# Optimization experiments

Hardware: AMD Instinct MI355X
Metric: run time of the kernel (lower is better)

Reference implementation:

```python
import jax, jax.numpy as jnp
import numpy as np

EMB = 1024
HID = 4 * EMB
HEADS = 16
HEAD_DIM = EMB // HEADS


def gelu_tanh(x):
    c = jnp.sqrt(jnp.asarray(2.0 / jnp.pi, x.dtype))
    return 0.5 * x * (1.0 + jnp.tanh(c * (x + 0.044715 * x ** 3)))


def layernorm(x, scale, shift, eps=1e-5):
    mean = jnp.mean(x, axis=-1, keepdims=True)
    var = jnp.var(x, axis=-1, keepdims=True)
    return scale * (x - mean) / jnp.sqrt(var + eps) + shift


def setup_inputs() -> dict:
    key = jax.random.key(0)
    ks = jax.random.split(key, 12)
    s = 0.02
    return {
        "x": jax.random.normal(ks[0], (2, 2048, EMB), jnp.float32),
        "Wq": jax.random.normal(ks[1], (EMB, EMB), jnp.float32) * s,
        "Wk": jax.random.normal(ks[2], (EMB, EMB), jnp.float32) * s,
        "Wv": jax.random.normal(ks[3], (EMB, EMB), jnp.float32) * s,
        "Wo": jax.random.normal(ks[4], (EMB, EMB), jnp.float32) * s,
        "bo": jnp.zeros((EMB,), jnp.float32),
        "W1": jax.random.normal(ks[5], (EMB, HID), jnp.float32) * s,
        "b1": jnp.zeros((HID,), jnp.float32),
        "W2": jax.random.normal(ks[6], (HID, EMB), jnp.float32) * s,
        "b2": jnp.zeros((EMB,), jnp.float32),
        "ln1_scale": jnp.ones((EMB,), jnp.float32),
        "ln1_shift": jnp.zeros((EMB,), jnp.float32),
        "ln2_scale": jnp.ones((EMB,), jnp.float32),
        "ln2_shift": jnp.zeros((EMB,), jnp.float32),
    }


def reference(x, Wq, Wk, Wv, Wo, bo, W1, b1, W2, b2,
              ln1_scale, ln1_shift, ln2_scale, ln2_shift):
    B, S, D = x.shape

    # pre-norm attention + residual
    h = layernorm(x, ln1_scale, ln1_shift)
    q = (h @ Wq).reshape(B, S, HEADS, HEAD_DIM).transpose(0, 2, 1, 3)  # bhsd
    k = (h @ Wk).reshape(B, S, HEADS, HEAD_DIM).transpose(0, 2, 1, 3)
    v = (h @ Wv).reshape(B, S, HEADS, HEAD_DIM).transpose(0, 2, 1, 3)

    scores = jnp.einsum("bhqd,bhkd->bhqk", q, k)
    causal = jnp.tril(jnp.ones((S, S), bool))
    scores = jnp.where(causal, scores, -jnp.inf)
    attn = jax.nn.softmax(scores / jnp.sqrt(jnp.asarray(HEAD_DIM, x.dtype)), axis=-1)
    ctx = jnp.einsum("bhqk,bhkd->bhqd", attn, v)
    ctx = ctx.transpose(0, 2, 1, 3).reshape(B, S, D)
    x = x + (ctx @ Wo + bo)

    # pre-norm FFN + residual
    h = layernorm(x, ln2_scale, ln2_shift)
    h = gelu_tanh(h @ W1 + b1) @ W2 + b2
    return x + h
```

## Files before the change

kernel.cpp:

```cpp
#include <hip/hip_runtime.h>
#include <hip/hip_bf16.h>
#include <stdint.h>

#define B_   2
#define S_   2048
#define D_   1024
#define H_   16
#define DH_  64
#define HID_ 4096
#define M_   4096

typedef __bf16 bf16x8 __attribute__((ext_vector_type(8)));
typedef float  f32x4  __attribute__((ext_vector_type(4)));

typedef const uint32_t __attribute__((address_space(1))) u32g;
typedef uint32_t       __attribute__((address_space(3))) u32l;

__device__ __forceinline__ uint16_t f2bf(float f) {
  uint32_t u = __builtin_bit_cast(uint32_t, f);
  u += 0x7FFFu + ((u >> 16) & 1u);
  return (uint16_t)(u >> 16);
}

__device__ __forceinline__ float bf2f(uint16_t u) {
  return __builtin_bit_cast(float, (uint32_t)u << 16);
}

__device__ __forceinline__ void gload_lds16(const void* g, void* l) {
  __builtin_amdgcn_global_load_lds((u32g*)g, (u32l*)l, 16, 0, 0);
}

__device__ __forceinline__ const bf16x8* lds8p(const uint16_t* base, int row,
                                               int cole) {
  int byt = (cole * 2) ^ ((row & 7) << 4);
  return reinterpret_cast<const bf16x8*>(base + row * 64 + (byt >> 1));
}

__global__ void wconv_t(const float* __restrict__ W, uint16_t* __restrict__ WT,
                        int K, int N) {
  __shared__ float tile[32][33];
  int n0 = blockIdx.x * 32, k0 = blockIdx.y * 32;
  int tx = threadIdx.x, ty = threadIdx.y;
#pragma unroll
  for (int i = 0; i < 4; ++i)
    tile[ty + i * 8][tx] = W[(size_t)(k0 + ty + i * 8) * N + n0 + tx];
  __syncthreads();
#pragma unroll
  for (int i = 0; i < 4; ++i)
    WT[(size_t)(n0 + ty + i * 8) * K + k0 + tx] = f2bf(tile[tx][ty + i * 8]);
}

__global__ __launch_bounds__(256) void ln_k(const float* __restrict__ x,
                                            const float* __restrict__ sc,
                                            const float* __restrict__ sh,
                                            uint16_t* __restrict__ out) {
  int row = blockIdx.x;
  int t = threadIdx.x;
  float4 v = reinterpret_cast<const float4*>(x + (size_t)row * D_)[t];
  float s = v.x + v.y + v.z + v.w;
  float ss = v.x * v.x + v.y * v.y + v.z * v.z + v.w * v.w;
#pragma unroll
  for (int off = 32; off >= 1; off >>= 1) {
    s += __shfl_xor(s, off);
    ss += __shfl_xor(ss, off);
  }
  __shared__ float red[8];
  int wid = t >> 6, lane = t & 63;
  if (lane == 0) { red[wid] = s; red[wid + 4] = ss; }
  __syncthreads();
  s = red[0] + red[1] + red[2] + red[3];
  ss = red[4] + red[5] + red[6] + red[7];
  float mean = s * (1.0f / D_);
  float var = ss * (1.0f / D_) - mean * mean;
  float rstd = rsqrtf(var + 1e-5f);
  float4 g = reinterpret_cast<const float4*>(sc)[t];
  float4 b = reinterpret_cast<const float4*>(sh)[t];
  ushort4 o;
  o.x = f2bf(g.x * (v.x - mean) * rstd + b.x);
  o.y = f2bf(g.y * (v.y - mean) * rstd + b.y);
  o.z = f2bf(g.z * (v.z - mean) * rstd + b.z);
  o.w = f2bf(g.w * (v.w - mean) * rstd + b.w);
  reinterpret_cast<ushort4*>(out + (size_t)row * D_)[t] = o;
}

__global__ __launch_bounds__(256) void reduce4_k(
    const uint16_t* __restrict__ P0, const uint16_t* __restrict__ P1,
    const uint16_t* __restrict__ P2, const uint16_t* __restrict__ P3,
    const float* __restrict__ resid, const float* __restrict__ bias,
    float* __restrict__ out) {
  int row = blockIdx.x, t = threadIdx.x;
  size_t base = (size_t)row * D_ + t * 4;
  float4 r = *reinterpret_cast<const float4*>(resid + base);
  float4 b = reinterpret_cast<const float4*>(bias)[t];
  ushort4 u0 = *reinterpret_cast<const ushort4*>(P0 + base);
  ushort4 u1 = *reinterpret_cast<const ushort4*>(P1 + base);
  ushort4 u2 = *reinterpret_cast<const ushort4*>(P2 + base);
  ushort4 u3 = *reinterpret_cast<const ushort4*>(P3 + base);
  float4 o;
  o.x = r.x + b.x + bf2f(u0.x) + bf2f(u1.x) + bf2f(u2.x) + bf2f(u3.x);
  o.y = r.y + b.y + bf2f(u0.y) + bf2f(u1.y) + bf2f(u2.y) + bf2f(u3.y);
  o.z = r.z + b.z + bf2f(u0.z) + bf2f(u1.z) + bf2f(u2.z) + bf2f(u3.z);
  o.w = r.w + b.w + bf2f(u0.w) + bf2f(u1.w) + bf2f(u2.w) + bf2f(u3.w);
  *reinterpret_cast<float4*>(out + base) = o;
}

__global__ void vtrans_k(const uint16_t* __restrict__ V, uint16_t* __restrict__ VT) {
  __shared__ uint16_t tile[32][33];
  int s0 = blockIdx.x * 32, d0 = blockIdx.y * 32, bh = blockIdx.z;
  int tx = threadIdx.x, ty = threadIdx.y;
  const uint16_t* vb = V + (size_t)bh * S_ * DH_;
  uint16_t* vtb = VT + (size_t)bh * DH_ * S_;
#pragma unroll
  for (int i = 0; i < 4; ++i)
    tile[ty + i * 8][tx] = vb[(size_t)(s0 + ty + i * 8) * DH_ + d0 + tx];
  __syncthreads();
#pragma unroll
  for (int i = 0; i < 4; ++i)
    vtb[(size_t)(d0 + ty + i * 8) * S_ + s0 + tx] = tile[tx][ty + i * 8];
}

template <int EPI>
__global__ __launch_bounds__(512, 2) void gemm8(
    const uint16_t* __restrict__ A, const uint16_t* __restrict__ BT,
    void* __restrict__ Cout, const float* __restrict__ bias,
    uint16_t* __restrict__ P0, uint16_t* __restrict__ P1,
    uint16_t* __restrict__ P2, uint16_t* __restrict__ P3,
    int M, int N, int K) {
  __shared__ uint16_t As[2][2][128 * 64];
  __shared__ uint16_t Bs[2][2][128 * 64];
  int t = threadIdx.x;
  int lane = t & 63, wid = t >> 6;
  int wm = wid >> 2, wn = wid & 3;
  int l15 = lane & 15, lk8 = (lane >> 4) * 8, lr4 = (lane >> 4) * 4;
  int gx = gridDim.x;
  int nwg = gx * gridDim.y;
  int bid = blockIdx.y * gx + blockIdx.x;
  int swz = (bid & 7) * (nwg >> 3) + (bid >> 3);
  int bx = swz % gx, by = swz / gx;
  int m0 = by * 256, n0 = bx * 256;
  int ksz = K / gridDim.z;
  int kbeg = blockIdx.z * ksz;
  int NT = ksz >> 6;

  int r0 = t >> 3, slot0 = t & 7;
  int scol = (slot0 ^ (r0 & 7)) * 8;

  auto STAGE_A = [&](int kt, int half, int buf) {
    const uint16_t* src =
        A + (size_t)(m0 + half * 128 + r0) * K + kbeg + kt * 64 + scol;
    uint16_t* dst = &As[buf][half][t * 8];
    gload_lds16(src, dst);
    gload_lds16(src + (size_t)64 * K, dst + 4096);
  };
  auto STAGE_B = [&](int kt, int half, int buf) {
    const uint16_t* src =
        BT + (size_t)(n0 + half * 128 + r0) * K + kbeg + kt * 64 + scol;
    uint16_t* dst = &Bs[buf][half][t * 8];
    gload_lds16(src, dst);
    gload_lds16(src + (size_t)64 * K, dst + 4096);
  };

  bf16x8 a[4][2], b[2][2];
  auto LDA = [&](int buf, int mh) {
#pragma unroll
    for (int j = 0; j < 4; ++j)
#pragma unroll
      for (int kk = 0; kk < 2; ++kk)
        a[j][kk] = *lds8p(As[buf][mh], wm * 64 + j * 16 + l15, kk * 32 + lk8);
  };
  auto LDB = [&](int buf, int nh) {
#pragma unroll
    for (int jj = 0; jj < 2; ++jj)
#pragma unroll
      for (int kk = 0; kk < 2; ++kk)
        b[jj][kk] = *lds8p(Bs[buf][nh], wn * 32 + jj * 16 + l15, kk * 32 + lk8);
  };

  f32x4 acc[8][4] = {};
  auto MM = [&](int mh, int nh) {
    __builtin_amdgcn_s_setprio(1);
#pragma unroll
    for (int kk = 0; kk < 2; ++kk)
#pragma unroll
      for (int j = 0; j < 4; ++j)
#pragma unroll
        for (int jj = 0; jj < 2; ++jj)
          acc[mh * 4 + j][nh * 2 + jj] = __builtin_amdgcn_mfma_f32_16x16x32_bf16(
              a[j][kk], b[jj][kk], acc[mh * 4 + j][nh * 2 + jj], 0, 0, 0);
    __builtin_amdgcn_s_setprio(0);
  };
  auto BAR = [&]() {
    __builtin_amdgcn_s_barrier();
    asm volatile("" ::: "memory");
  };
  auto LGKM0 = [&]() {
    asm volatile("s_waitcnt lgkmcnt(0)" ::: "memory");
    __builtin_amdgcn_sched_barrier(0);
  };

  STAGE_A(0, 0, 0);
  STAGE_B(0, 1, 0);
  STAGE_B(0, 0, 0);
  STAGE_A(0, 1, 0);
  STAGE_A(1, 0, 1);
  STAGE_B(1, 1, 1);
  asm volatile("s_waitcnt vmcnt(4)" ::: "memory");
  BAR();

  for (int T = 0; T < NT; ++T) {
    int cur = T & 1;
    LDA(cur, 0);
    LDB(cur, 0);
    if (T + 1 < NT) STAGE_B(T + 1, 0, cur ^ 1);
    BAR(); LGKM0();
    MM(0, 0);
    BAR();
    LDB(cur, 1);
    if (T + 1 < NT) STAGE_A(T + 1, 1, cur ^ 1);
    BAR(); LGKM0();
    MM(0, 1);
    BAR();
    LDA(cur, 1);
    if (T + 2 < NT) STAGE_A(T + 2, 0, cur);
    BAR(); LGKM0();
    MM(1, 1);
    BAR();
    LDB(cur, 0);
    if (T + 2 < NT) STAGE_B(T + 2, 1, cur);
    BAR(); LGKM0();
    MM(1, 0);
    if (T + 1 < NT) {
      if (T == NT - 2) {
        asm volatile("s_waitcnt vmcnt(0)" ::: "memory");
      } else {
        asm volatile("s_waitcnt vmcnt(4)" ::: "memory");
      }
    }
    BAR();
  }

  uint16_t* Pz = nullptr;
  if constexpr (EPI == 3) {
    int z = blockIdx.z;
    Pz = (z == 0) ? P0 : (z == 1) ? P1 : (z == 2) ? P2 : P3;
  }
#pragma unroll
  for (int mi = 0; mi < 8; ++mi) {
#pragma unroll
    for (int ni = 0; ni < 4; ++ni) {
#pragma unroll
      for (int rr = 0; rr < 4; ++rr) {
        int gm = m0 + (mi >> 2) * 128 + wm * 64 + (mi & 3) * 16 + lr4 + rr;
        int gn = n0 + (ni >> 1) * 128 + wn * 32 + (ni & 1) * 16 + l15;
        float v = acc[mi][ni][rr];
        if constexpr (EPI == 0) {
          int which = gn >> 10, nc = gn & 1023;
          int h = nc >> 6, dh = nc & 63;
          int bb = gm >> 11, s = gm & 2047;
          ((uint16_t*)Cout)[((size_t)which * 32 + bb * 16 + h) * (S_ * 64) +
                            (size_t)s * 64 + dh] = f2bf(v);
        } else if constexpr (EPI == 2) {
          float u = v + bias[gn];
          float y = 0.7978845608028654f * (u + 0.044715f * u * u * u);
          float e = __expf(2.0f * y);
          float th = 1.0f - 2.0f / (e + 1.0f);
          ((uint16_t*)Cout)[(size_t)gm * N + gn] = f2bf(0.5f * u * (1.0f + th));
        } else {
          Pz[(size_t)gm * N + gn] = f2bf(v);
        }
      }
    }
  }
}

template <int EPI>
__global__ __launch_bounds__(256) void gemm_bt(
    const uint16_t* __restrict__ A, const uint16_t* __restrict__ BT,
    void* __restrict__ Cout, const float* __restrict__ bias,
    const float* __restrict__ resid, int M, int N, int K) {
  __shared__ uint16_t Asm_[128 * 64];
  __shared__ uint16_t Bsm_[128 * 64];
  int t = threadIdx.x;
  int lane = t & 63, wid = t >> 6;
  int wr = wid >> 1, wc = wid & 1;
  int nwg = gridDim.x * gridDim.y;
  int bid = blockIdx.y * gridDim.x + blockIdx.x;
  int swz = (bid & 7) * (nwg >> 3) + (bid >> 3);
  int bx = swz % gridDim.x, by = swz / gridDim.x;
  int m0 = by * 128, n0 = bx * 128;
  int l15 = lane & 15, lk8 = (lane >> 4) * 8;
  f32x4 acc[4][4] = {};

  auto STAGE = [&](int k0) {
#pragma unroll
    for (int it = 0; it < 4; ++it) {
      int idx = it * 256 + t;
      int r = idx >> 3, slot = idx & 7;
      int c = (slot ^ (r & 7)) * 8;
      gload_lds16(A + (size_t)(m0 + r) * K + k0 + c, &Asm_[idx * 8]);
      gload_lds16(BT + (size_t)(n0 + r) * K + k0 + c, &Bsm_[idx * 8]);
    }
  };

  int niter = K >> 6;
  for (int ki = 0; ki < niter; ++ki) {
    __syncthreads();
    STAGE(ki * 64);
    __syncthreads();
#pragma unroll
    for (int kk = 0; kk < 2; ++kk) {
      bf16x8 a[4], b[4];
#pragma unroll
      for (int mi = 0; mi < 4; ++mi)
        a[mi] = *lds8p(Asm_, wr * 64 + mi * 16 + l15, kk * 32 + lk8);
#pragma unroll
      for (int ni = 0; ni < 4; ++ni)
        b[ni] = *lds8p(Bsm_, wc * 64 + ni * 16 + l15, kk * 32 + lk8);
#pragma unroll
      for (int mi = 0; mi < 4; ++mi)
#pragma unroll
        for (int ni = 0; ni < 4; ++ni)
          acc[mi][ni] = __builtin_amdgcn_mfma_f32_16x16x32_bf16(
              a[mi], b[ni], acc[mi][ni], 0, 0, 0);
    }
  }
  int lr4 = (lane >> 4) * 4;
#pragma unroll
  for (int mi = 0; mi < 4; ++mi) {
#pragma unroll
    for (int ni = 0; ni < 4; ++ni) {
#pragma unroll
      for (int r = 0; r < 4; ++r) {
        int gm = m0 + wr * 64 + mi * 16 + lr4 + r;
        int gn = n0 + wc * 64 + ni * 16 + l15;
        float v = acc[mi][ni][r];
        if constexpr (EPI == 1) {
          ((float*)Cout)[(size_t)gm * N + gn] =
              resid[(size_t)gm * N + gn] + v + bias[gn];
        }
      }
    }
  }
}

__global__ __launch_bounds__(256) void attn_k(const uint16_t* __restrict__ Q,
                                              const uint16_t* __restrict__ Kv,
                                              const uint16_t* __restrict__ VT,
                                              uint16_t* __restrict__ ctx) {
  __shared__ uint16_t Ksm[2][64 * 64];
  __shared__ uint16_t Vsm[2][64 * 64];
  __shared__ uint16_t Psm[4][16 * 64];
  int bh = blockIdx.y;
  int t = threadIdx.x, lane = t & 63, wid = t >> 6;
  int l15 = lane & 15, lk8 = (lane >> 4) * 8, lr4 = (lane >> 4) * 4;

  auto STAGE = [&](int kt, int bufi) {
    int k0 = kt * 64;
#pragma unroll
    for (int it = 0; it < 2; ++it) {
      int idx = it * 256 + t;
      int r = idx >> 3, slot = idx & 7;
      int c = (slot ^ (r & 7)) * 8;
      gload_lds16(Kv + ((size_t)bh * S_ + k0 + r) * 64 + c, &Ksm[bufi][idx * 8]);
      gload_lds16(VT + ((size_t)bh * 64 + r) * S_ + k0 + c, &Vsm[bufi][idx * 8]);
    }
  };

  for (int half = 0; half < 2; ++half) {
    int qt = half ? 31 - blockIdx.x : blockIdx.x;
    int q0 = qt * 64;
    bf16x8 qf[2];
#pragma unroll
    for (int kk = 0; kk < 2; ++kk)
      qf[kk] = *reinterpret_cast<const bf16x8*>(
          &Q[((size_t)bh * S_ + q0 + wid * 16 + l15) * 64 + kk * 32 + lk8]);
    f32x4 o[4] = {};
    float mrow[4], lsum[4];
#pragma unroll
    for (int r = 0; r < 4; ++r) { mrow[r] = -3.0e38f; lsum[r] = 0.0f; }

    int nkt = qt + 1;
    STAGE(0, 0);
    for (int kt = 0; kt < nkt; ++kt) {
      int cur = kt & 1;
      if (kt + 1 < nkt) {
        STAGE(kt + 1, cur ^ 1);
        asm volatile("s_waitcnt vmcnt(4)" ::: "memory");
      } else {
        asm volatile("s_waitcnt vmcnt(0)" ::: "memory");
      }
      __builtin_amdgcn_s_barrier();
      asm volatile("" ::: "memory");
      __builtin_amdgcn_sched_barrier(0);
      const uint16_t* Kb = Ksm[cur];
      const uint16_t* Vb = Vsm[cur];

      f32x4 sf[4] = {};
#pragma unroll
      for (int kk = 0; kk < 2; ++kk)
#pragma unroll
        for (int nt = 0; nt < 4; ++nt) {
          bf16x8 kb = *lds8p(Kb, nt * 16 + l15, kk * 32 + lk8);
          sf[nt] = __builtin_amdgcn_mfma_f32_16x16x32_bf16(qf[kk], kb, sf[nt], 0, 0, 0);
        }
      float sv[4][4];
      if (kt == qt) {
#pragma unroll
        for (int nt = 0; nt < 4; ++nt)
#pragma unroll
          for (int r = 0; r < 4; ++r) {
            float s = sf[nt][r] * 0.125f;
            int key = nt * 16 + l15;
            int qr = wid * 16 + lr4 + r;
            sv[nt][r] = (key <= qr) ? s : -3.0e38f;
          }
      } else {
#pragma unroll
        for (int nt = 0; nt < 4; ++nt)
#pragma unroll
          for (int r = 0; r < 4; ++r) sv[nt][r] = sf[nt][r] * 0.125f;
      }
      float pmax[4];
#pragma unroll
      for (int r = 0; r < 4; ++r)
        pmax[r] = fmaxf(fmaxf(sv[0][r], sv[1][r]), fmaxf(sv[2][r], sv[3][r]));
#pragma unroll
      for (int off = 8; off >= 1; off >>= 1)
#pragma unroll
        for (int r = 0; r < 4; ++r)
          pmax[r] = fmaxf(pmax[r], __shfl_xor(pmax[r], off));
      float fac[4];
#pragma unroll
      for (int r = 0; r < 4; ++r) {
        float mn = fmaxf(mrow[r], pmax[r]);
        fac[r] = __expf(mrow[r] - mn);
        mrow[r] = mn;
        lsum[r] *= fac[r];
      }
#pragma unroll
      for (int dt = 0; dt < 4; ++dt)
#pragma unroll
        for (int r = 0; r < 4; ++r) o[dt][r] *= fac[r];
      float psum[4] = {0.0f, 0.0f, 0.0f, 0.0f};
#pragma unroll
      for (int nt = 0; nt < 4; ++nt)
#pragma unroll
        for (int r = 0; r < 4; ++r) {
          float p = __expf(sv[nt][r] - mrow[r]);
          psum[r] += p;
          int prow = lr4 + r, pcol = nt * 16 + l15;
          Psm[wid][prow * 64 + ((((pcol * 2) ^ ((prow & 7) << 4))) >> 1)] = f2bf(p);
        }
#pragma unroll
      for (int off = 8; off >= 1; off >>= 1)
#pragma unroll
        for (int r = 0; r < 4; ++r) psum[r] += __shfl_xor(psum[r], off);
#pragma unroll
      for (int r = 0; r < 4; ++r) lsum[r] += psum[r];
#pragma unroll
      for (int kk = 0; kk < 2; ++kk) {
        bf16x8 pa = *lds8p(Psm[wid], l15, kk * 32 + lk8);
#pragma unroll
        for (int dt = 0; dt < 4; ++dt) {
          bf16x8 vb = *lds8p(Vb, dt * 16 + l15, kk * 32 + lk8);
          o[dt] = __builtin_amdgcn_mfma_f32_16x16x32_bf16(pa, vb, o[dt], 0, 0, 0);
        }
      }
      asm volatile("s_waitcnt lgkmcnt(0)" ::: "memory");
      __builtin_amdgcn_sched_barrier(0);
      __builtin_amdgcn_s_barrier();
      asm volatile("" ::: "memory");
    }
    int b = bh >> 4, h = bh & 15;
#pragma unroll
    for (int dt = 0; dt < 4; ++dt)
#pragma unroll
      for (int r = 0; r < 4; ++r) {
        int s = q0 + wid * 16 + lr4 + r;
        int dh = dt * 16 + l15;
        ctx[((size_t)(b * S_ + s)) * D_ + h * 64 + dh] = f2bf(o[dt][r] / lsum[r]);
      }
  }
}

extern "C" void kernel_launch(void* const* d_in, const int* in_sizes, int n_in,
                              void* d_out, int out_size, void* d_ws, size_t ws_size,
                              hipStream_t stream) {
  const float* x    = (const float*)d_in[0];
  const float* Wq   = (const float*)d_in[1];
  const float* Wk   = (const float*)d_in[2];
  const float* Wv   = (const float*)d_in[3];
  const float* Wo   = (const float*)d_in[4];
  const float* bo   = (const float*)d_in[5];
  const float* W1   = (const float*)d_in[6];
  const float* b1   = (const float*)d_in[7];
  const float* W2   = (const float*)d_in[8];
  const float* b2   = (const float*)d_in[9];
  const float* ln1s = (const float*)d_in[10];
  const float* ln1b = (const float*)d_in[11];
  const float* ln2s = (const float*)d_in[12];
  const float* ln2b = (const float*)d_in[13];
  float* out = (float*)d_out;
  char* ws = (char*)d_ws;

  const size_t MB = 1024 * 1024;
  uint16_t* WQKVT = (uint16_t*)(ws + 0);
  uint16_t* WOT   = (uint16_t*)(ws + 6 * MB);
  uint16_t* W1T   = (uint16_t*)(ws + 8 * MB);
  uint16_t* W2T   = (uint16_t*)(ws + 16 * MB);
  uint16_t* H1    = (uint16_t*)(ws + 24 * MB);
  float*    X1    = (float*)(ws + 32 * MB);
  uint16_t* QKV   = (uint16_t*)(ws + 48 * MB);
  uint16_t* VTb   = (uint16_t*)(ws + 72 * MB);
  uint16_t* CTX   = (uint16_t*)(ws + 80 * MB);
  uint16_t* FFH   = (uint16_t*)(ws + 48 * MB);
  uint16_t* SP0   = (uint16_t*)(ws + 0);
  uint16_t* SP1   = (uint16_t*)(ws + 8 * MB);
  uint16_t* SP2   = (uint16_t*)(ws + 24 * MB);
  uint16_t* SP3   = (uint16_t*)(ws + 80 * MB);

  dim3 b32x8(32, 8);
  wconv_t<<<dim3(32, 32), b32x8, 0, stream>>>(Wq, WQKVT, 1024, 1024);
  wconv_t<<<dim3(32, 32), b32x8, 0, stream>>>(Wk, WQKVT + 1024 * 1024, 1024, 1024);
  wconv_t<<<dim3(32, 32), b32x8, 0, stream>>>(Wv, WQKVT + 2 * 1024 * 1024, 1024, 1024);
  wconv_t<<<dim3(32, 32), b32x8, 0, stream>>>(Wo, WOT, 1024, 1024);
  wconv_t<<<dim3(128, 32), b32x8, 0, stream>>>(W1, W1T, 1024, 4096);
  wconv_t<<<dim3(32, 128), b32x8, 0, stream>>>(W2, W2T, 4096, 1024);

  ln_k<<<M_, 256, 0, stream>>>(x, ln1s, ln1b, H1);
  gemm8<0><<<dim3(12, 16), 512, 0, stream>>>(H1, WQKVT, QKV, nullptr,
                                             nullptr, nullptr, nullptr, nullptr,
                                             M_, 3072, 1024);
  const uint16_t* Qp = QKV;
  const uint16_t* Kp = QKV + (size_t)32 * S_ * 64;
  const uint16_t* Vp = QKV + (size_t)64 * S_ * 64;
  vtrans_k<<<dim3(64, 2, 32), b32x8, 0, stream>>>(Vp, VTb);
  attn_k<<<dim3(16, 32), 256, 0, stream>>>(Qp, Kp, VTb, CTX);
  gemm_bt<1><<<dim3(8, 32), 256, 0, stream>>>(CTX, WOT, X1, bo, x, M_, 1024, 1024);
  ln_k<<<M_, 256, 0, stream>>>(X1, ln2s, ln2b, H1);
  gemm8<2><<<dim3(16, 16), 512, 0, stream>>>(H1, W1T, FFH, b1,
                                             nullptr, nullptr, nullptr, nullptr,
                                             M_, 4096, 1024);
  gemm8<3><<<dim3(4, 16, 4), 512, 0, stream>>>(FFH, W2T, nullptr, nullptr,
                                               SP0, SP1, SP2, SP3,
                                               M_, 1024, 4096);
  reduce4_k<<<M_, 256, 0, stream>>>(SP0, SP1, SP2, SP3, X1, b2, out);
}
```

Baseline: 265.5 us.

## Rewrite attention as single-wave 32x32 MFMA kernel with register-resident P

Replaces the 4-wave, 64-row-tile attention kernel with a one-wave-per-block kernel over 32-query tiles using 32x32x16 MFMAs. S is computed transposed so each lane owns one query column, and P is packed to bf16 and moved between half-waves with cvt_pk and permlane32_swap instead of going through LDS. The softmax scale and log2(e) are folded into K in the QKV GEMM epilogue so the kernel can use exp2 directly. The running-max rescale is skipped unless the max grows by more than 8. The changes aim to cut LDS traffic, barriers and per-element exp/scale work, and to raise block count for load balance, at the cost of less K/V reuse per block.

```diff
diff --git a/kernel.cpp b/kernel.cpp
--- a/kernel.cpp
+++ b/kernel.cpp
@@ -12,9 +12,13 @@
 
 typedef __bf16 bf16x8 __attribute__((ext_vector_type(8)));
 typedef float  f32x4  __attribute__((ext_vector_type(4)));
+typedef float  f32x16 __attribute__((ext_vector_type(16)));
+typedef uint32_t u32x4v __attribute__((ext_vector_type(4)));
 
 typedef const uint32_t __attribute__((address_space(1))) u32g;
 typedef uint32_t       __attribute__((address_space(3))) u32l;
+
+#define SCL2K_ 0.18033688011112042f
 
 __device__ __forceinline__ uint16_t f2bf(float f) {
   uint32_t u = __builtin_bit_cast(uint32_t, f);
@@ -34,6 +38,15 @@
                                                int cole) {
   int byt = (cole * 2) ^ ((row & 7) << 4);
   return reinterpret_cast<const bf16x8*>(base + row * 64 + (byt >> 1));
+}
+
+__device__ __forceinline__ uint32_t cvtpk_bf16(float lo, float hi) {
+  uint32_t d;
+  asm("v_cvt_pk_bf16_f32 %0, %1, %2" : "=v"(d) : "v"(lo), "v"(hi));
+  return d;
+}
+__device__ __forceinline__ void pl32swap(uint32_t& a, uint32_t& b) {
+  asm volatile("v_permlane32_swap_b32 %0, %1" : "+v"(a), "+v"(b));
 }
 
 __global__ void wconv_t(const float* __restrict__ W, uint16_t* __restrict__ WT,
@@ -257,6 +270,7 @@
           int which = gn >> 10, nc = gn & 1023;
           int h = nc >> 6, dh = nc & 63;
           int bb = gm >> 11, s = gm & 2047;
+          if (which == 1) v *= SCL2K_;
           ((uint16_t*)Cout)[((size_t)which * 32 + bb * 16 + h) * (S_ * 64) +
                             (size_t)s * 64 + dh] = f2bf(v);
         } else if constexpr (EPI == 2) {
@@ -343,143 +357,135 @@
   }
 }
 
-__global__ __launch_bounds__(256) void attn_k(const uint16_t* __restrict__ Q,
-                                              const uint16_t* __restrict__ Kv,
-                                              const uint16_t* __restrict__ VT,
-                                              uint16_t* __restrict__ ctx) {
-  __shared__ uint16_t Ksm[2][64 * 64];
-  __shared__ uint16_t Vsm[2][64 * 64];
-  __shared__ uint16_t Psm[4][16 * 64];
-  int bh = blockIdx.y;
-  int t = threadIdx.x, lane = t & 63, wid = t >> 6;
-  int l15 = lane & 15, lk8 = (lane >> 4) * 8, lr4 = (lane >> 4) * 4;
-
-  auto STAGE = [&](int kt, int bufi) {
-    int k0 = kt * 64;
-#pragma unroll
-    for (int it = 0; it < 2; ++it) {
-      int idx = it * 256 + t;
-      int r = idx >> 3, slot = idx & 7;
-      int c = (slot ^ (r & 7)) * 8;
-      gload_lds16(Kv + ((size_t)bh * S_ + k0 + r) * 64 + c, &Ksm[bufi][idx * 8]);
-      gload_lds16(VT + ((size_t)bh * 64 + r) * S_ + k0 + c, &Vsm[bufi][idx * 8]);
-    }
-  };
+__global__ __launch_bounds__(64) void attn32_k(const uint16_t* __restrict__ Q,
+                                               const uint16_t* __restrict__ Kv,
+                                               const uint16_t* __restrict__ VT,
+                                               uint16_t* __restrict__ ctx) {
+  __shared__ uint16_t Ksm[2][32 * 64];
+  __shared__ uint16_t Vsm[2][32 * 64];
+  __shared__ float invLDS[2][32];
+  int bid = blockIdx.x;
+  int wgrp = bid >> 3;
+  int j = wgrp & 31;
+  int bh = (bid & 7) + 8 * (wgrp >> 5);
+  int lane = threadIdx.x;
+  int l31 = lane & 31, lh = lane >> 5;
+  int b_ = bh >> 4, h_ = bh & 15;
+
+  auto STAGE = [&](int k0, int bufi) {
+#pragma unroll
+    for (int c = 0; c < 4; ++c) {
+      int idx = c * 64 + lane;
+      int r = idx >> 3, sl = idx & 7;
+      int slp = sl ^ (r & 7);
+      gload_lds16(Kv + ((size_t)bh * S_ + k0 + r) * 64 + slp * 8,
+                  &Ksm[bufi][idx * 8]);
+      int dh = 2 * r + (slp >> 2), ko = (slp & 3) * 8;
+      gload_lds16(VT + ((size_t)bh * 64 + dh) * S_ + k0 + ko,
+                  &Vsm[bufi][idx * 8]);
+    }
+  };
+
+  int buf = 0;
+  STAGE(0, 0);
 
   for (int half = 0; half < 2; ++half) {
-    int qt = half ? 31 - blockIdx.x : blockIdx.x;
-    int q0 = qt * 64;
-    bf16x8 qf[2];
-#pragma unroll
-    for (int kk = 0; kk < 2; ++kk)
-      qf[kk] = *reinterpret_cast<const bf16x8*>(
-          &Q[((size_t)bh * S_ + q0 + wid * 16 + l15) * 64 + kk * 32 + lk8]);
-    f32x4 o[4] = {};
-    float mrow[4], lsum[4];
-#pragma unroll
-    for (int r = 0; r < 4; ++r) { mrow[r] = -3.0e38f; lsum[r] = 0.0f; }
-
+    int qt = half ? (63 - j) : j;
     int nkt = qt + 1;
-    STAGE(0, 0);
-    for (int kt = 0; kt < nkt; ++kt) {
-      int cur = kt & 1;
-      if (kt + 1 < nkt) {
-        STAGE(kt + 1, cur ^ 1);
-        asm volatile("s_waitcnt vmcnt(4)" ::: "memory");
+    int qbase = qt * 32;
+    bf16x8 qf[4];
+#pragma unroll
+    for (int dk = 0; dk < 4; ++dk)
+      qf[dk] = *reinterpret_cast<const bf16x8*>(
+          Q + ((size_t)bh * S_ + qbase + l31) * 64 + dk * 16 + lh * 8);
+    f32x16 o0 = {}, o1 = {};
+    float mrow = -3.0e38f, lsum = 0.0f;
+
+    for (int t = 0; t < nkt; ++t) {
+      if (t + 1 < nkt) {
+        STAGE((t + 1) * 32, buf ^ 1);
+        asm volatile("s_waitcnt vmcnt(8)" ::: "memory");
+      } else if (half == 0) {
+        STAGE(0, buf ^ 1);
+        asm volatile("s_waitcnt vmcnt(8)" ::: "memory");
       } else {
         asm volatile("s_waitcnt vmcnt(0)" ::: "memory");
       }
-      __builtin_amdgcn_s_barrier();
-      asm volatile("" ::: "memory");
       __builtin_amdgcn_sched_barrier(0);
-      const uint16_t* Kb = Ksm[cur];
-      const uint16_t* Vb = Vsm[cur];
-
-      f32x4 sf[4] = {};
-#pragma unroll
-      for (int kk = 0; kk < 2; ++kk)
-#pragma unroll
-        for (int nt = 0; nt < 4; ++nt) {
-          bf16x8 kb = *lds8p(Kb, nt * 16 + l15, kk * 32 + lk8);
-          sf[nt] = __builtin_amdgcn_mfma_f32_16x16x32_bf16(qf[kk], kb, sf[nt], 0, 0, 0);
+      f32x16 Sf = {};
+#pragma unroll
+      for (int dk = 0; dk < 4; ++dk) {
+        bf16x8 kf = *lds8p(Ksm[buf], l31, dk * 16 + lh * 8);
+        Sf = __builtin_amdgcn_mfma_f32_32x32x16_bf16(kf, qf[dk], Sf, 0, 0, 0);
+      }
+      float sv[16];
+      if (t == nkt - 1) {
+#pragma unroll
+        for (int rr = 0; rr < 16; ++rr) {
+          int koff = (rr & 3) + 8 * (rr >> 2) + 4 * lh;
+          sv[rr] = (koff <= l31) ? Sf[rr] : -3.0e38f;
         }
-      float sv[4][4];
-      if (kt == qt) {
-#pragma unroll
-        for (int nt = 0; nt < 4; ++nt)
-#pragma unroll
-          for (int r = 0; r < 4; ++r) {
-            float s = sf[nt][r] * 0.125f;
-            int key = nt * 16 + l15;
-            int qr = wid * 16 + lr4 + r;
-            sv[nt][r] = (key <= qr) ? s : -3.0e38f;
-          }
       } else {
 #pragma unroll
-        for (int nt = 0; nt < 4; ++nt)
-#pragma unroll
-          for (int r = 0; r < 4; ++r) sv[nt][r] = sf[nt][r] * 0.125f;
-      }
-      float pmax[4];
-#pragma unroll
-      for (int r = 0; r < 4; ++r)
-        pmax[r] = fmaxf(fmaxf(sv[0][r], sv[1][r]), fmaxf(sv[2][r], sv[3][r]));
-#pragma unroll
-      for (int off = 8; off >= 1; off >>= 1)
-#pragma unroll
-        for (int r = 0; r < 4; ++r)
-          pmax[r] = fmaxf(pmax[r], __shfl_xor(pmax[r], off));
-      float fac[4];
-#pragma unroll
-      for (int r = 0; r < 4; ++r) {
-        float mn = fmaxf(mrow[r], pmax[r]);
-        fac[r] = __expf(mrow[r] - mn);
-        mrow[r] = mn;
-        lsum[r] *= fac[r];
-      }
-#pragma unroll
-      for (int dt = 0; dt < 4; ++dt)
-#pragma unroll
-        for (int r = 0; r < 4; ++r) o[dt][r] *= fac[r];
-      float psum[4] = {0.0f, 0.0f, 0.0f, 0.0f};
-#pragma unroll
-      for (int nt = 0; nt < 4; ++nt)
-#pragma unroll
-        for (int r = 0; r < 4; ++r) {
-          float p = __expf(sv[nt][r] - mrow[r]);
-          psum[r] += p;
-          int prow = lr4 + r, pcol = nt * 16 + l15;
-          Psm[wid][prow * 64 + ((((pcol * 2) ^ ((prow & 7) << 4))) >> 1)] = f2bf(p);
-        }
-#pragma unroll
-      for (int off = 8; off >= 1; off >>= 1)
-#pragma unroll
-        for (int r = 0; r < 4; ++r) psum[r] += __shfl_xor(psum[r], off);
-#pragma unroll
-      for (int r = 0; r < 4; ++r) lsum[r] += psum[r];
-#pragma unroll
-      for (int kk = 0; kk < 2; ++kk) {
-        bf16x8 pa = *lds8p(Psm[wid], l15, kk * 32 + lk8);
-#pragma unroll
-        for (int dt = 0; dt < 4; ++dt) {
-          bf16x8 vb = *lds8p(Vb, dt * 16 + l15, kk * 32 + lk8);
-          o[dt] = __builtin_amdgcn_mfma_f32_16x16x32_bf16(pa, vb, o[dt], 0, 0, 0);
-        }
-      }
-      asm volatile("s_waitcnt lgkmcnt(0)" ::: "memory");
-      __builtin_amdgcn_sched_barrier(0);
-      __builtin_amdgcn_s_barrier();
-      asm volatile("" ::: "memory");
-    }
-    int b = bh >> 4, h = bh & 15;
-#pragma unroll
-    for (int dt = 0; dt < 4; ++dt)
-#pragma unroll
-      for (int r = 0; r < 4; ++r) {
-        int s = q0 + wid * 16 + lr4 + r;
-        int dh = dt * 16 + l15;
-        ctx[((size_t)(b * S_ + s)) * D_ + h * 64 + dh] = f2bf(o[dt][r] / lsum[r]);
-      }
+        for (int rr = 0; rr < 16; ++rr) sv[rr] = Sf[rr];
+      }
+      float mt = sv[0];
+#pragma unroll
+      for (int rr = 1; rr < 16; ++rr) mt = fmaxf(mt, sv[rr]);
+#pragma unroll
+      for (int off = 32; off >= 1; off >>= 1)
+        mt = fmaxf(mt, __shfl_xor(mt, off));
+      if (mt > mrow + 8.0f) {
+        float fac = __builtin_amdgcn_exp2f(mrow - mt);
+        mrow = mt;
+        lsum *= fac;
+#pragma unroll
+        for (int rr = 0; rr < 16; ++rr) { o0[rr] *= fac; o1[rr] *= fac; }
+      }
+      float pv[16];
+#pragma unroll
+      for (int rr = 0; rr < 16; ++rr) {
+        pv[rr] = __builtin_amdgcn_exp2f(sv[rr] - mrow);
+        lsum += pv[rr];
+      }
+      uint32_t a0 = cvtpk_bf16(pv[0], pv[1]), b0 = cvtpk_bf16(pv[4], pv[5]);
+      pl32swap(a0, b0);
+      uint32_t a1 = cvtpk_bf16(pv[2], pv[3]), b1 = cvtpk_bf16(pv[6], pv[7]);
+      pl32swap(a1, b1);
+      u32x4v w0 = {a0, a1, b0, b1};
+      bf16x8 pa0 = __builtin_bit_cast(bf16x8, w0);
+      uint32_t a2 = cvtpk_bf16(pv[8], pv[9]), b2 = cvtpk_bf16(pv[12], pv[13]);
+      pl32swap(a2, b2);
+      uint32_t a3 = cvtpk_bf16(pv[10], pv[11]), b3 = cvtpk_bf16(pv[14], pv[15]);
+      pl32swap(a3, b3);
+      u32x4v w1 = {a2, a3, b2, b3};
+      bf16x8 pa1 = __builtin_bit_cast(bf16x8, w1);
+      int vrow = l31 >> 1, vcb = (l31 & 1) * 32 + lh * 8;
+      bf16x8 v00 = *lds8p(Vsm[buf], vrow, vcb);
+      o0 = __builtin_amdgcn_mfma_f32_32x32x16_bf16(pa0, v00, o0, 0, 0, 0);
+      bf16x8 v01 = *lds8p(Vsm[buf], vrow, vcb + 16);
+      o0 = __builtin_amdgcn_mfma_f32_32x32x16_bf16(pa1, v01, o0, 0, 0, 0);
+      bf16x8 v10 = *lds8p(Vsm[buf], 16 + vrow, vcb);
+      o1 = __builtin_amdgcn_mfma_f32_32x32x16_bf16(pa0, v10, o1, 0, 0, 0);
+      bf16x8 v11 = *lds8p(Vsm[buf], 16 + vrow, vcb + 16);
+      o1 = __builtin_amdgcn_mfma_f32_32x32x16_bf16(pa1, v11, o1, 0, 0, 0);
+      buf ^= 1;
+    }
+    lsum += __shfl_xor(lsum, 32);
+    if (lane < 32) invLDS[half][l31] = 1.0f / lsum;
+    asm volatile("s_waitcnt lgkmcnt(0)" ::: "memory");
+    __builtin_amdgcn_sched_barrier(0);
+    float inv[16];
+#pragma unroll
+    for (int rr = 0; rr < 16; ++rr)
+      inv[rr] = invLDS[half][(rr & 3) + 8 * (rr >> 2) + 4 * lh];
+#pragma unroll
+    for (int rr = 0; rr < 16; ++rr) {
+      int s = qbase + (rr & 3) + 8 * (rr >> 2) + 4 * lh;
+      size_t base = ((size_t)(b_ * S_ + s)) * D_ + h_ * 64;
+      ctx[base + l31] = f2bf(o0[rr] * inv[rr]);
+      ctx[base + 32 + l31] = f2bf(o1[rr] * inv[rr]);
+    }
   }
 }
 
@@ -535,7 +541,7 @@
   const uint16_t* Kp = QKV + (size_t)32 * S_ * 64;
   const uint16_t* Vp = QKV + (size_t)64 * S_ * 64;
   vtrans_k<<<dim3(64, 2, 32), b32x8, 0, stream>>>(Vp, VTb);
-  attn_k<<<dim3(16, 32), 256, 0, stream>>>(Qp, Kp, VTb, CTX);
+  attn32_k<<<dim3(1024), 64, 0, stream>>>(Qp, Kp, VTb, CTX);
   gemm_bt<1><<<dim3(8, 32), 256, 0, stream>>>(CTX, WOT, X1, bo, x, M_, 1024, 1024);
   ln_k<<<M_, 256, 0, stream>>>(X1, ln2s, ln2b, H1);
   gemm8<2><<<dim3(16, 16), 512, 0, stream>>>(H1, W1T, FFH, b1,
```

Measured after the change: 269.7 us. No clear change (+1.6%).
